# Kernel tuning notes

Hardware: AMD Instinct MI355X
Metric: run time of the kernel (lower is better)

Reference implementation:

```python
import jax, jax.numpy as jnp
import numpy as np
from jax import lax

B = 16384
T = 16

def _lin(x, w, b):
    return x @ w.T + b

def setup_inputs() -> dict:
    key = jax.random.key(0)
    ks = jax.random.split(key, 24)
    d = {
        'x': jax.random.normal(ks[0], (T, B, 64), jnp.float32),
        'cue': jax.random.uniform(ks[1], (B,), jnp.float32),
        'hc1': jax.random.normal(ks[2], (B, 256), jnp.float32),
        'hc2': jax.random.normal(ks[3], (B, 256), jnp.float32),
        'hc3': jax.random.normal(ks[4], (B, 256), jnp.float32),
        'hc4': jax.random.normal(ks[5], (B, 256), jnp.float32),
    }
    def w(k, o, i):
        return jax.random.normal(k, (o, i), jnp.float32) * 0.05
    def b(k, o):
        return jax.random.normal(k, (o,), jnp.float32) * 0.05
    d.update({
        'w1_i2h': w(ks[6], 256, 64),  'b1_i2h': b(ks[7], 256),
        'w1_h2h': w(ks[8], 256, 256), 'b1_h2h': b(ks[9], 256),
        'w1_h2o': w(ks[10], 64, 256), 'b1_h2o': b(ks[11], 64),
        'w2_i2h': w(ks[12], 256, 64), 'b2_i2h': b(ks[13], 256),
        'w2_h2h': w(ks[14], 256, 256),'b2_h2h': b(ks[15], 256),
        'w2_h2o': w(ks[16], 64, 256), 'b2_h2o': b(ks[17], 64),
        'w3_i2h': w(ks[18], 256, 130),'b3_i2h': b(ks[19], 256),
        'w3_h2h': w(ks[20], 256, 256),'b3_h2h': b(ks[21], 256),
        'w3_h2o': w(ks[22], 64, 256), 'b3_h2o': b(ks[23], 64),
        'w_fc': jax.random.normal(jax.random.fold_in(key, 100), (2, 64), jnp.float32) * 0.05,
        'b_fc': jax.random.normal(jax.random.fold_in(key, 101), (2,), jnp.float32) * 0.05,
    })
    return d

def reference(x, cue, hc1, hc2, hc3, hc4,
              w1_i2h, b1_i2h, w1_h2h, b1_h2h, w1_h2o, b1_h2o,
              w2_i2h, b2_i2h, w2_h2h, b2_h2h, w2_h2o, b2_h2o,
              w3_i2h, b3_i2h, w3_h2h, b3_h2h, w3_h2o, b3_h2o,
              w_fc, b_fc):
    # cue channels are identical at every timestep
    cue_step = jnp.stack([cue * 10.0, 10.0 * jnp.abs(cue - 1.0)], axis=-1)  # [B,2]
    cue_arr = jnp.broadcast_to(cue_step, (T,) + cue_step.shape)             # [T,B,2]

    def step(carry, xt):
        h1, h2, h3 = carry
        h1 = jnp.tanh(_lin(xt, w1_i2h, b1_i2h) + _lin(h1, w1_h2h, b1_h2h))
        o1 = jnp.tanh(_lin(h1, w1_h2o, b1_h2o))
        h2 = jnp.tanh(_lin(xt, w2_i2h, b2_i2h) + _lin(h2, w2_h2h, b2_h2h))
        o2 = jnp.tanh(_lin(h2, w2_h2o, b2_h2o))
        mid = jnp.concatenate([cue_step, o1, o2], axis=-1)  # [B,130]
        h3 = jnp.tanh(_lin(mid, w3_i2h, b3_i2h) + _lin(h3, w3_h2h, b3_h2h))
        of = jax.nn.relu(_lin(h3, w3_h2o, b3_h2o))
        y = _lin(of, w_fc, b_fc)
        return (h1, h2, h3), (y, o1, o2, of)

    (h1, h2, h3), (ys, o1s, o2s, ofs) = lax.scan(step, (hc1, hc2, hc3), x)
    # feed1_arr/feed2_arr are torch.empty (never written); use zeros as deterministic stand-in
    feed = jnp.zeros((T, x.shape[1], 256), dtype=x.dtype)
    return (ys, h1, h2, h3, hc4, o1s, o2s, cue_arr, feed, feed, ofs)
```

## Files before the change

### kernel.cpp

```cpp
#include <hip/hip_runtime.h>
#include <stdint.h>
#include <stddef.h>


#define BN 16384
#define TT 16

typedef short s16x8 __attribute__((ext_vector_type(8)));
typedef short s16x4 __attribute__((ext_vector_type(4)));
typedef float f32x4 __attribute__((ext_vector_type(4)));

#define MFMA(a, b, c) __builtin_amdgcn_mfma_f32_16x16x32_bf16((a), (b), (c), 0, 0, 0)
#define BARL() asm volatile("s_waitcnt lgkmcnt(0)\n\ts_barrier" ::: "memory")

__device__ __forceinline__ short f2bf(float f) {
  union { float f; uint32_t u; } v; v.f = f;
  uint32_t u = v.u;
  u += 0x7FFFu + ((u >> 16) & 1u);
  return (short)(u >> 16);
}
__device__ __forceinline__ float bf2f(short s) {
  union { uint32_t u; float f; } v; v.u = ((uint32_t)(uint16_t)s) << 16;
  return v.f;
}
__device__ __forceinline__ float fast_tanh(float xx) {
  float x = fminf(8.f, fmaxf(-8.f, xx));
  float e = __expf(2.f * x);
  return (e - 1.f) * __builtin_amdgcn_rcpf(e + 1.f);
}
__device__ __forceinline__ void nt_st4(float* p, f32x4 v) {
  __builtin_nontemporal_store(v, (f32x4*)p);
}
__device__ __forceinline__ f32x4 nt_ld4(const float* p) {
  return __builtin_nontemporal_load((const f32x4*)p);
}

struct PrepPtrs {
  const float *w1i, *w1h, *w1o, *w2i, *w2h, *w2o, *w3i, *w3h, *w3o;
  const float *b1i, *b1h, *b2i, *b2h, *b3i, *b3h, *bo1, *bo2, *bo3, *wfc, *bfc;
};

__global__ void prep_kernel(PrepPtrs pp, short* __restrict__ wpk, float* __restrict__ wmisc) {
  const float* P[9] = {pp.w1i, pp.w1h, pp.w1o, pp.w2i, pp.w2h, pp.w2o, pp.w3i, pp.w3h, pp.w3o};
  const int LD_[9] = {64, 256, 256, 64, 256, 256, 130, 256, 256};
  const int C0_[9] = {0, 0, 0, 0, 0, 0, 2, 0, 0};
  const int NT_[9] = {16, 16, 4, 16, 16, 4, 16, 16, 4};
  const int DO_[10] = {0, 16384, 81920, 98304, 114688, 180224, 196608, 229376, 294912, 311296};
  int stride = gridDim.x * blockDim.x;
  for (int g = blockIdx.x * blockDim.x + threadIdx.x; g < 311296; g += stride) {
    int m = 0;
    while (g >= DO_[m + 1]) ++m;
    int p = g - DO_[m];
    int NT = NT_[m];
    int frag = p >> 9, lane = (p >> 3) & 63, e = p & 7;
    int kt = frag / NT, nt = frag - kt * NT;
    int row = nt * 16 + (lane & 15);
    int col = kt * 32 + ((lane >> 4) << 3) + e;
    wpk[g] = f2bf(P[m][(size_t)row * LD_[m] + C0_[m] + col]);
  }
  for (int i = blockIdx.x * blockDim.x + threadIdx.x; i < 1602; i += stride) {
    float v;
    if      (i < 256)  v = pp.b1i[i]         + pp.b1h[i];
    else if (i < 512)  v = pp.b2i[i - 256]   + pp.b2h[i - 256];
    else if (i < 768)  v = pp.b3i[i - 512]   + pp.b3h[i - 512];
    else if (i < 832)  v = pp.bo1[i - 768];
    else if (i < 896)  v = pp.bo2[i - 832];
    else if (i < 960)  v = pp.bo3[i - 896];
    else if (i < 1088) v = pp.wfc[i - 960];
    else if (i < 1090) v = pp.bfc[i - 1088];
    else if (i < 1346) v = pp.w3i[(size_t)(i - 1090) * 130];
    else               v = pp.w3i[(size_t)(i - 1346) * 130 + 1];
    wmisc[i] = v;
  }
}

__launch_bounds__(512, 2)
__global__ void rnn_main(const float* __restrict__ x, const float* __restrict__ cue,
                         const float* __restrict__ hc1, const float* __restrict__ hc2,
                         const float* __restrict__ hc3, const float* __restrict__ hc4,
                         const short* __restrict__ wpk, const float* __restrict__ wmisc,
                         float* __restrict__ out) {
  __shared__ __align__(16) char pool[141312];
  short* h1s  = (short*)pool;
  short* h2s  = (short*)(pool + 32768);
  short* h3s  = (short*)(pool + 65536);
  short* o12s = (short*)(pool + 98304);
  float* ofl  = (float*)(pool + 114688);
  short* hscr = (short*)(pool + 98304);
  short* xls  = (short*)(pool + 133120);
  __shared__ float cue0[64], cue1[64];
  __shared__ __align__(16) float misc[1604];

  const int tid = threadIdx.x;
  const int wv = tid >> 6;
  const int lane = tid & 63;
  const int lr = lane & 15;
  const int lq = lane >> 4;
  const int swz = (lr & 7) << 3;
  const int r0 = blockIdx.x * 64;

  float* out_ys  = out;
  float* out_h1  = out + 524288;
  float* out_h2  = out + 4718592;
  float* out_h3  = out + 8912896;
  float* out_h4  = out + 13107200;
  float* out_o1s = out + 17301504;
  float* out_o2s = out + 34078720;
  float* out_cue = out + 50855936;
  float* out_f1  = out + 51380224;
  float* out_f2  = out + 118489088;
  float* out_of  = out + 185597952;

  for (int i = tid; i < 1602; i += 512) misc[i] = wmisc[i];
  if (tid < 64) {
    float cv = cue[r0 + tid];
    cue0[tid] = cv * 10.f;
    cue1[tid] = 10.f * fabsf(cv - 1.f);
  }
  for (int i = tid; i < 4096; i += 512) {
    int r = i >> 6, c0 = (i & 63) << 2;
    int li = r * 256 + (c0 ^ ((r & 7) << 3));
    size_t g = (size_t)(r0 + r) * 256 + c0;
    f32x4 v1 = __builtin_nontemporal_load((const f32x4*)(hc1 + g));
    f32x4 v2 = __builtin_nontemporal_load((const f32x4*)(hc2 + g));
    f32x4 v3 = __builtin_nontemporal_load((const f32x4*)(hc3 + g));
    f32x4 v4 = __builtin_nontemporal_load((const f32x4*)(hc4 + g));
    *(s16x4*)&h1s[li] = (s16x4){f2bf(v1.x), f2bf(v1.y), f2bf(v1.z), f2bf(v1.w)};
    *(s16x4*)&h2s[li] = (s16x4){f2bf(v2.x), f2bf(v2.y), f2bf(v2.z), f2bf(v2.w)};
    *(s16x4*)&h3s[li] = (s16x4){f2bf(v3.x), f2bf(v3.y), f2bf(v3.z), f2bf(v3.w)};
    nt_st4(out_h4 + g, v4);
  }
  const int xr = tid >> 3, xcq = (tid & 7) << 3;
  {
    const float* px = x + ((size_t)(r0 + xr)) * 64 + xcq;
    f32x4 a0 = nt_ld4(px);
    f32x4 a1 = nt_ld4(px + 4);
    *(s16x8*)&xls[xr * 64 + (xcq ^ ((xr & 7) << 3))] =
        (s16x8){f2bf(a0.x), f2bf(a0.y), f2bf(a0.z), f2bf(a0.w),
                f2bf(a1.x), f2bf(a1.y), f2bf(a1.z), f2bf(a1.w)};
  }
  __syncthreads();

  const short* Wp1i  = wpk;
  const short* Wp1h  = wpk + 16384;
  const short* Wp1o  = wpk + 81920;
  const short* Wp2i  = wpk + 98304;
  const short* Wp2h  = wpk + 114688;
  const short* Wp2o  = wpk + 180224;
  const short* Wp3ab = wpk + 196608;
  const short* Wp3h  = wpk + 229376;
  const short* Wp3o  = wpk + 294912;
  const float* bh1v = misc;
  const float* bh2v = misc + 256;
  const float* bh3v = misc + 512;
  const float* bo1v = misc + 768;
  const float* bo2v = misc + 832;
  const float* bofv = misc + 896;
  const float* wfcv = misc + 960;
  const float* bfcv = misc + 1088;
  const float* w3c0 = misc + 1090;
  const float* w3c1 = misc + 1346;

  for (int t = 0; t < TT; ++t) {
    BARL();

    {
      f32x4 acc1[4][2];
      #pragma unroll
      for (int j = 0; j < 2; ++j) {
        int nb = (2 * wv + j) * 16 + lq * 4;
        f32x4 b1 = *(const f32x4*)(bh1v + nb);
        #pragma unroll
        for (int rt = 0; rt < 4; ++rt) acc1[rt][j] = b1;
      }
      #pragma unroll
      for (int kt = 0; kt < 2; ++kt) {
        s16x8 aw0 = *(const s16x8*)(Wp1i + ((size_t)(kt * 16 + 2 * wv) * 64 + lane) * 8);
        s16x8 aw1 = *(const s16x8*)(Wp1i + ((size_t)(kt * 16 + 2 * wv + 1) * 64 + lane) * 8);
        #pragma unroll
        for (int rt = 0; rt < 4; ++rt) {
          s16x8 xb = *(const s16x8*)&xls[(rt * 16 + lr) * 64 + ((kt * 32 + lq * 8) ^ swz)];
          acc1[rt][0] = MFMA(aw0, xb, acc1[rt][0]);
          acc1[rt][1] = MFMA(aw1, xb, acc1[rt][1]);
        }
      }
      #pragma unroll
      for (int kt = 0; kt < 8; ++kt) {
        s16x8 aw0 = *(const s16x8*)(Wp1h + ((size_t)(kt * 16 + 2 * wv) * 64 + lane) * 8);
        s16x8 aw1 = *(const s16x8*)(Wp1h + ((size_t)(kt * 16 + 2 * wv + 1) * 64 + lane) * 8);
        #pragma unroll
        for (int rt = 0; rt < 4; ++rt) {
          s16x8 hb = *(const s16x8*)&h1s[(rt * 16 + lr) * 256 + ((kt * 32 + lq * 8) ^ swz)];
          acc1[rt][0] = MFMA(aw0, hb, acc1[rt][0]);
          acc1[rt][1] = MFMA(aw1, hb, acc1[rt][1]);
        }
      }
      #pragma unroll
      for (int j = 0; j < 2; ++j) {
        int cb = (2 * wv + j) * 16 + lq * 4;
        #pragma unroll
        for (int rt = 0; rt < 4; ++rt) {
          *(s16x4*)&hscr[(rt * 16 + lr) * 256 + (cb ^ swz)] =
              (s16x4){f2bf(fast_tanh(acc1[rt][j][0])), f2bf(fast_tanh(acc1[rt][j][1])),
                      f2bf(fast_tanh(acc1[rt][j][2])), f2bf(fast_tanh(acc1[rt][j][3]))};
        }
      }
    }

    {
      f32x4 acc2[4][2];
      #pragma unroll
      for (int j = 0; j < 2; ++j) {
        int nb = (2 * wv + j) * 16 + lq * 4;
        f32x4 b2 = *(const f32x4*)(bh2v + nb);
        #pragma unroll
        for (int rt = 0; rt < 4; ++rt) acc2[rt][j] = b2;
      }
      #pragma unroll
      for (int kt = 0; kt < 2; ++kt) {
        s16x8 aw0 = *(const s16x8*)(Wp2i + ((size_t)(kt * 16 + 2 * wv) * 64 + lane) * 8);
        s16x8 aw1 = *(const s16x8*)(Wp2i + ((size_t)(kt * 16 + 2 * wv + 1) * 64 + lane) * 8);
        #pragma unroll
        for (int rt = 0; rt < 4; ++rt) {
          s16x8 xb = *(const s16x8*)&xls[(rt * 16 + lr) * 64 + ((kt * 32 + lq * 8) ^ swz)];
          acc2[rt][0] = MFMA(aw0, xb, acc2[rt][0]);
          acc2[rt][1] = MFMA(aw1, xb, acc2[rt][1]);
        }
      }
      #pragma unroll
      for (int kt = 0; kt < 8; ++kt) {
        s16x8 aw0 = *(const s16x8*)(Wp2h + ((size_t)(kt * 16 + 2 * wv) * 64 + lane) * 8);
        s16x8 aw1 = *(const s16x8*)(Wp2h + ((size_t)(kt * 16 + 2 * wv + 1) * 64 + lane) * 8);
        #pragma unroll
        for (int rt = 0; rt < 4; ++rt) {
          s16x8 hb = *(const s16x8*)&h2s[(rt * 16 + lr) * 256 + ((kt * 32 + lq * 8) ^ swz)];
          acc2[rt][0] = MFMA(aw0, hb, acc2[rt][0]);
          acc2[rt][1] = MFMA(aw1, hb, acc2[rt][1]);
        }
      }
      __syncthreads();
      #pragma unroll
      for (int j = 0; j < 2; ++j) {
        int cb = (2 * wv + j) * 16 + lq * 4;
        #pragma unroll
        for (int rt = 0; rt < 4; ++rt) {
          *(s16x4*)&h2s[(rt * 16 + lr) * 256 + (cb ^ swz)] =
              (s16x4){f2bf(fast_tanh(acc2[rt][j][0])), f2bf(fast_tanh(acc2[rt][j][1])),
                      f2bf(fast_tanh(acc2[rt][j][2])), f2bf(fast_tanh(acc2[rt][j][3]))};
        }
      }
      #pragma unroll
      for (int i = 0; i < 4; ++i) {
        int e = (i * 512 + tid) * 8;
        *(s16x8*)&h1s[e] = *(const s16x8*)&hscr[e];
      }
      __syncthreads();
    }

    {
      int cell = wv >> 2, w4 = wv & 3;
      const short* hs = cell ? h2s : h1s;
      const short* Wo = cell ? Wp2o : Wp1o;
      const float* bo = cell ? bo2v : bo1v;
      int nb = w4 * 16 + lq * 4;
      f32x4 bb = *(const f32x4*)(bo + nb);
      f32x4 acc[4];
      #pragma unroll
      for (int rt = 0; rt < 4; ++rt) acc[rt] = bb;
      #pragma unroll
      for (int kt = 0; kt < 8; ++kt) {
        s16x8 aw = *(const s16x8*)(Wo + ((size_t)(kt * 4 + w4) * 64 + lane) * 8);
        #pragma unroll
        for (int rt = 0; rt < 4; ++rt) {
          s16x8 hb = *(const s16x8*)&hs[(rt * 16 + lr) * 256 + ((kt * 32 + lq * 8) ^ swz)];
          acc[rt] = MFMA(aw, hb, acc[rt]);
        }
      }
      int cb = cell * 64 + nb;
      #pragma unroll
      for (int rt = 0; rt < 4; ++rt) {
        *(s16x4*)&o12s[(rt * 16 + lr) * 128 + (cb ^ swz)] =
            (s16x4){f2bf(fast_tanh(acc[rt][0])), f2bf(fast_tanh(acc[rt][1])),
                    f2bf(fast_tanh(acc[rt][2])), f2bf(fast_tanh(acc[rt][3]))};
      }
    }
    __syncthreads();

    {
      f32x4 acc3[4][2];
      #pragma unroll
      for (int j = 0; j < 2; ++j) {
        int nb = (2 * wv + j) * 16 + lq * 4;
        f32x4 bb  = *(const f32x4*)(bh3v + nb);
        f32x4 c0w = *(const f32x4*)(w3c0 + nb);
        f32x4 c1w = *(const f32x4*)(w3c1 + nb);
        #pragma unroll
        for (int rt = 0; rt < 4; ++rt) {
          float cz = cue0[rt * 16 + lr], co = cue1[rt * 16 + lr];
          acc3[rt][j] = bb + cz * c0w + co * c1w;
        }
      }
      #pragma unroll
      for (int kt = 0; kt < 4; ++kt) {
        s16x8 aw0 = *(const s16x8*)(Wp3ab + ((size_t)(kt * 16 + 2 * wv) * 64 + lane) * 8);
        s16x8 aw1 = *(const s16x8*)(Wp3ab + ((size_t)(kt * 16 + 2 * wv + 1) * 64 + lane) * 8);
        #pragma unroll
        for (int rt = 0; rt < 4; ++rt) {
          s16x8 ob = *(const s16x8*)&o12s[(rt * 16 + lr) * 128 + ((kt * 32 + lq * 8) ^ swz)];
          acc3[rt][0] = MFMA(aw0, ob, acc3[rt][0]);
          acc3[rt][1] = MFMA(aw1, ob, acc3[rt][1]);
        }
      }
      #pragma unroll
      for (int kt = 0; kt < 8; ++kt) {
        s16x8 aw0 = *(const s16x8*)(Wp3h + ((size_t)(kt * 16 + 2 * wv) * 64 + lane) * 8);
        s16x8 aw1 = *(const s16x8*)(Wp3h + ((size_t)(kt * 16 + 2 * wv + 1) * 64 + lane) * 8);
        #pragma unroll
        for (int rt = 0; rt < 4; ++rt) {
          s16x8 hb = *(const s16x8*)&h3s[(rt * 16 + lr) * 256 + ((kt * 32 + lq * 8) ^ swz)];
          acc3[rt][0] = MFMA(aw0, hb, acc3[rt][0]);
          acc3[rt][1] = MFMA(aw1, hb, acc3[rt][1]);
        }
      }
      __syncthreads();
      #pragma unroll
      for (int j = 0; j < 2; ++j) {
        int cb = (2 * wv + j) * 16 + lq * 4;
        #pragma unroll
        for (int rt = 0; rt < 4; ++rt) {
          *(s16x4*)&h3s[(rt * 16 + lr) * 256 + (cb ^ swz)] =
              (s16x4){f2bf(fast_tanh(acc3[rt][j][0])), f2bf(fast_tanh(acc3[rt][j][1])),
                      f2bf(fast_tanh(acc3[rt][j][2])), f2bf(fast_tanh(acc3[rt][j][3]))};
        }
      }
      __syncthreads();
    }

    int tn = (t + 1 < TT) ? (t + 1) : t;
    const float* pxn = x + ((size_t)tn * BN + r0 + xr) * 64 + xcq;
    f32x4 xa0 = nt_ld4(pxn);
    f32x4 xa1 = nt_ld4(pxn + 4);

    if (wv < 4) {
      int nb = wv * 16 + lq * 4;
      f32x4 bb = *(const f32x4*)(bofv + nb);
      f32x4 acc[4];
      #pragma unroll
      for (int rt = 0; rt < 4; ++rt) acc[rt] = bb;
      #pragma unroll
      for (int kt = 0; kt < 8; ++kt) {
        s16x8 aw = *(const s16x8*)(Wp3o + ((size_t)(kt * 4 + wv) * 64 + lane) * 8);
        #pragma unroll
        for (int rt = 0; rt < 4; ++rt) {
          s16x8 hb = *(const s16x8*)&h3s[(rt * 16 + lr) * 256 + ((kt * 32 + lq * 8) ^ swz)];
          acc[rt] = MFMA(aw, hb, acc[rt]);
        }
      }
      #pragma unroll
      for (int rt = 0; rt < 4; ++rt) {
        f32x4 v = (f32x4){fmaxf(0.f, acc[rt][0]), fmaxf(0.f, acc[rt][1]),
                          fmaxf(0.f, acc[rt][2]), fmaxf(0.f, acc[rt][3])};
        *(f32x4*)&ofl[(rt * 16 + lr) * 72 + nb] = v;
      }
    } else {
      size_t ob = ((size_t)t * BN + r0) * 64;
      float* targ = (wv < 6) ? out_o1s : out_o2s;
      int coff = (wv < 6) ? 0 : 64;
      int wq = wv & 1;
      #pragma unroll
      for (int s = 0; s < 8; ++s) {
        int f = wq * 2048 + s * 256 + lane * 4;
        int r = f >> 6, c = f & 63;
        s16x4 v = *(const s16x4*)&o12s[r * 128 + ((c + coff) ^ ((r & 7) << 3))];
        nt_st4(targ + ob + f, (f32x4){bf2f(v[0]), bf2f(v[1]), bf2f(v[2]), bf2f(v[3])});
      }
    }
    BARL();

    {
      size_t ob = ((size_t)t * BN + r0) * 64;
      int r = tid >> 3, c0 = (tid & 7) << 3;
      nt_st4(out_of + ob + r * 64 + c0,     *(const f32x4*)&ofl[r * 72 + c0]);
      nt_st4(out_of + ob + r * 64 + c0 + 4, *(const f32x4*)&ofl[r * 72 + c0 + 4]);
      *(s16x8*)&xls[xr * 64 + (xcq ^ ((xr & 7) << 3))] =
          (s16x8){f2bf(xa0.x), f2bf(xa0.y), f2bf(xa0.z), f2bf(xa0.w),
                  f2bf(xa1.x), f2bf(xa1.y), f2bf(xa1.z), f2bf(xa1.w)};
      if (tid < 128) {
        int rr = tid >> 1, jj = tid & 1;
        const f32x4* wr4 = (const f32x4*)(wfcv + jj * 64);
        const f32x4* or4 = (const f32x4*)&ofl[rr * 72];
        f32x4 sv = (f32x4){0.f, 0.f, 0.f, 0.f};
        #pragma unroll
        for (int kk = 0; kk < 16; ++kk) sv += or4[kk] * wr4[kk];
        float s = bfcv[jj] + sv[0] + sv[1] + sv[2] + sv[3];
        size_t yi = ((size_t)t * BN + r0 + rr) * 2 + jj;
        __builtin_nontemporal_store(s, out_ys + yi);
        __builtin_nontemporal_store(jj ? cue1[rr] : cue0[rr], out_cue + yi);
      }
      size_t fb = ((size_t)t * BN + r0) * 256;
      f32x4 z = (f32x4){0.f, 0.f, 0.f, 0.f};
      #pragma unroll
      for (int s = 0; s < 8; ++s) {
        nt_st4(out_f1 + fb + (size_t)(s * 512 + tid) * 4, z);
        nt_st4(out_f2 + fb + (size_t)(s * 512 + tid) * 4, z);
      }
    }
  }

  for (int i = tid; i < 4096; i += 512) {
    int r = i >> 6, c0 = (i & 63) << 2;
    int li = r * 256 + (c0 ^ ((r & 7) << 3));
    size_t g = (size_t)(r0 + r) * 256 + c0;
    s16x4 s1 = *(const s16x4*)&h1s[li];
    s16x4 s2 = *(const s16x4*)&h2s[li];
    s16x4 s3 = *(const s16x4*)&h3s[li];
    nt_st4(out_h1 + g, (f32x4){bf2f(s1[0]), bf2f(s1[1]), bf2f(s1[2]), bf2f(s1[3])});
    nt_st4(out_h2 + g, (f32x4){bf2f(s2[0]), bf2f(s2[1]), bf2f(s2[2]), bf2f(s2[3])});
    nt_st4(out_h3 + g, (f32x4){bf2f(s3[0]), bf2f(s3[1]), bf2f(s3[2]), bf2f(s3[3])});
  }
}

extern "C" void kernel_launch(void* const* d_in, const int* in_sizes, int n_in,
                              void* d_out, int out_size, void* d_ws, size_t ws_size,
                              hipStream_t stream) {
  const float* x   = (const float*)d_in[0];
  const float* cue = (const float*)d_in[1];
  const float* hc1 = (const float*)d_in[2];
  const float* hc2 = (const float*)d_in[3];
  const float* hc3 = (const float*)d_in[4];
  const float* hc4 = (const float*)d_in[5];
  PrepPtrs pp;
  pp.w1i = (const float*)d_in[6];  pp.b1i = (const float*)d_in[7];
  pp.w1h = (const float*)d_in[8];  pp.b1h = (const float*)d_in[9];
  pp.w1o = (const float*)d_in[10]; pp.bo1 = (const float*)d_in[11];
  pp.w2i = (const float*)d_in[12]; pp.b2i = (const float*)d_in[13];
  pp.w2h = (const float*)d_in[14]; pp.b2h = (const float*)d_in[15];
  pp.w2o = (const float*)d_in[16]; pp.bo2 = (const float*)d_in[17];
  pp.w3i = (const float*)d_in[18]; pp.b3i = (const float*)d_in[19];
  pp.w3h = (const float*)d_in[20]; pp.b3h = (const float*)d_in[21];
  pp.w3o = (const float*)d_in[22]; pp.bo3 = (const float*)d_in[23];
  pp.wfc = (const float*)d_in[24]; pp.bfc = (const float*)d_in[25];

  short* wpk   = (short*)d_ws;
  float* wmisc = (float*)((char*)d_ws + 622592);

  prep_kernel<<<64, 256, 0, stream>>>(pp, wpk, wmisc);
  rnn_main<<<256, 512, 0, stream>>>(x, cue, hc1, hc2, hc3, hc4, wpk, wmisc, (float*)d_out);
}
```

Before: 524.5 us.

## Fuse h3 recurrent GEMM into o1/o2 stage and drop a barrier

Moves the h3·W3h recurrent matmul, which depends only on the previous h3, into the o1/o2 output-projection loop so both run in one pass and interleave MFMAs. This removes one __syncthreads per timestep and lets the cell-3 stage finish with only the short input-projection part. It also simplifies tanh to a single-rcp form and uses the HIP bf16 conversion intrinsic, which may compile to hardware conversion. The tanh rewrite drops the lower clamp, so it relies on exp underflow behaving well for very negative inputs.

```diff
diff --git a/kernel.cpp b/kernel.cpp
--- a/kernel.cpp
+++ b/kernel.cpp
@@ -1,4 +1,5 @@
 #include <hip/hip_runtime.h>
+#include <hip/hip_bf16.h>
 #include <stdint.h>
 #include <stddef.h>
 
@@ -14,25 +15,28 @@
 #define BARL() asm volatile("s_waitcnt lgkmcnt(0)\n\ts_barrier" ::: "memory")
 
 __device__ __forceinline__ short f2bf(float f) {
-  union { float f; uint32_t u; } v; v.f = f;
-  uint32_t u = v.u;
-  u += 0x7FFFu + ((u >> 16) & 1u);
-  return (short)(u >> 16);
+  __hip_bfloat16 h = __float2bfloat16(f);
+  short s;
+  __builtin_memcpy(&s, &h, 2);
+  return s;
 }
 __device__ __forceinline__ float bf2f(short s) {
   union { uint32_t u; float f; } v; v.u = ((uint32_t)(uint16_t)s) << 16;
   return v.f;
 }
-__device__ __forceinline__ float fast_tanh(float xx) {
-  float x = fminf(8.f, fmaxf(-8.f, xx));
-  float e = __expf(2.f * x);
-  return (e - 1.f) * __builtin_amdgcn_rcpf(e + 1.f);
+__device__ __forceinline__ float fast_tanh(float x) {
+  float e = __expf(2.f * fminf(x, 8.f));
+  return 1.f - 2.f * __builtin_amdgcn_rcpf(e + 1.f);
 }
 __device__ __forceinline__ void nt_st4(float* p, f32x4 v) {
   __builtin_nontemporal_store(v, (f32x4*)p);
 }
 __device__ __forceinline__ f32x4 nt_ld4(const float* p) {
   return __builtin_nontemporal_load((const f32x4*)p);
+}
+__device__ __forceinline__ s16x4 tanh4bf(f32x4 a) {
+  return (s16x4){f2bf(fast_tanh(a[0])), f2bf(fast_tanh(a[1])),
+                 f2bf(fast_tanh(a[2])), f2bf(fast_tanh(a[3]))};
 }
 
 struct PrepPtrs {
@@ -125,9 +129,9 @@
     f32x4 v2 = __builtin_nontemporal_load((const f32x4*)(hc2 + g));
     f32x4 v3 = __builtin_nontemporal_load((const f32x4*)(hc3 + g));
     f32x4 v4 = __builtin_nontemporal_load((const f32x4*)(hc4 + g));
-    *(s16x4*)&h1s[li] = (s16x4){f2bf(v1.x), f2bf(v1.y), f2bf(v1.z), f2bf(v1.w)};
-    *(s16x4*)&h2s[li] = (s16x4){f2bf(v2.x), f2bf(v2.y), f2bf(v2.z), f2bf(v2.w)};
-    *(s16x4*)&h3s[li] = (s16x4){f2bf(v3.x), f2bf(v3.y), f2bf(v3.z), f2bf(v3.w)};
+    *(s16x4*)&h1s[li] = (s16x4){f2bf(v1[0]), f2bf(v1[1]), f2bf(v1[2]), f2bf(v1[3])};
+    *(s16x4*)&h2s[li] = (s16x4){f2bf(v2[0]), f2bf(v2[1]), f2bf(v2[2]), f2bf(v2[3])};
+    *(s16x4*)&h3s[li] = (s16x4){f2bf(v3[0]), f2bf(v3[1]), f2bf(v3[2]), f2bf(v3[3])};
     nt_st4(out_h4 + g, v4);
   }
   const int xr = tid >> 3, xcq = (tid & 7) << 3;
@@ -136,8 +140,8 @@
     f32x4 a0 = nt_ld4(px);
     f32x4 a1 = nt_ld4(px + 4);
     *(s16x8*)&xls[xr * 64 + (xcq ^ ((xr & 7) << 3))] =
-        (s16x8){f2bf(a0.x), f2bf(a0.y), f2bf(a0.z), f2bf(a0.w),
-                f2bf(a1.x), f2bf(a1.y), f2bf(a1.z), f2bf(a1.w)};
+        (s16x8){f2bf(a0[0]), f2bf(a0[1]), f2bf(a0[2]), f2bf(a0[3]),
+                f2bf(a1[0]), f2bf(a1[1]), f2bf(a1[2]), f2bf(a1[3])};
   }
   __syncthreads();
 
@@ -199,11 +203,8 @@
       for (int j = 0; j < 2; ++j) {
         int cb = (2 * wv + j) * 16 + lq * 4;
         #pragma unroll
-        for (int rt = 0; rt < 4; ++rt) {
-          *(s16x4*)&hscr[(rt * 16 + lr) * 256 + (cb ^ swz)] =
-              (s16x4){f2bf(fast_tanh(acc1[rt][j][0])), f2bf(fast_tanh(acc1[rt][j][1])),
-                      f2bf(fast_tanh(acc1[rt][j][2])), f2bf(fast_tanh(acc1[rt][j][3]))};
-        }
+        for (int rt = 0; rt < 4; ++rt)
+          *(s16x4*)&hscr[(rt * 16 + lr) * 256 + (cb ^ swz)] = tanh4bf(acc1[rt][j]);
       }
     }
 
@@ -243,11 +244,8 @@
       for (int j = 0; j < 2; ++j) {
         int cb = (2 * wv + j) * 16 + lq * 4;
         #pragma unroll
-        for (int rt = 0; rt < 4; ++rt) {
-          *(s16x4*)&h2s[(rt * 16 + lr) * 256 + (cb ^ swz)] =
-              (s16x4){f2bf(fast_tanh(acc2[rt][j][0])), f2bf(fast_tanh(acc2[rt][j][1])),
-                      f2bf(fast_tanh(acc2[rt][j][2])), f2bf(fast_tanh(acc2[rt][j][3]))};
-        }
+        for (int rt = 0; rt < 4; ++rt)
+          *(s16x4*)&h2s[(rt * 16 + lr) * 256 + (cb ^ swz)] = tanh4bf(acc2[rt][j]);
       }
       #pragma unroll
       for (int i = 0; i < 4; ++i) {
@@ -257,49 +255,51 @@
       __syncthreads();
     }
 
+    f32x4 acc3[4][2];
     {
+      #pragma unroll
+      for (int j = 0; j < 2; ++j) {
+        int nb = (2 * wv + j) * 16 + lq * 4;
+        f32x4 bb  = *(const f32x4*)(bh3v + nb);
+        f32x4 c0w = *(const f32x4*)(w3c0 + nb);
+        f32x4 c1w = *(const f32x4*)(w3c1 + nb);
+        #pragma unroll
+        for (int rt = 0; rt < 4; ++rt) {
+          float cz = cue0[rt * 16 + lr], co = cue1[rt * 16 + lr];
+          acc3[rt][j] = bb + cz * c0w + co * c1w;
+        }
+      }
       int cell = wv >> 2, w4 = wv & 3;
       const short* hs = cell ? h2s : h1s;
       const short* Wo = cell ? Wp2o : Wp1o;
       const float* bo = cell ? bo2v : bo1v;
       int nb = w4 * 16 + lq * 4;
       f32x4 bb = *(const f32x4*)(bo + nb);
-      f32x4 acc[4];
-      #pragma unroll
-      for (int rt = 0; rt < 4; ++rt) acc[rt] = bb;
+      f32x4 acco[4];
+      #pragma unroll
+      for (int rt = 0; rt < 4; ++rt) acco[rt] = bb;
       #pragma unroll
       for (int kt = 0; kt < 8; ++kt) {
-        s16x8 aw = *(const s16x8*)(Wo + ((size_t)(kt * 4 + w4) * 64 + lane) * 8);
-        #pragma unroll
-        for (int rt = 0; rt < 4; ++rt) {
-          s16x8 hb = *(const s16x8*)&hs[(rt * 16 + lr) * 256 + ((kt * 32 + lq * 8) ^ swz)];
-          acc[rt] = MFMA(aw, hb, acc[rt]);
+        s16x8 aw0 = *(const s16x8*)(Wp3h + ((size_t)(kt * 16 + 2 * wv) * 64 + lane) * 8);
+        s16x8 aw1 = *(const s16x8*)(Wp3h + ((size_t)(kt * 16 + 2 * wv + 1) * 64 + lane) * 8);
+        s16x8 awo = *(const s16x8*)(Wo + ((size_t)(kt * 4 + w4) * 64 + lane) * 8);
+        #pragma unroll
+        for (int rt = 0; rt < 4; ++rt) {
+          s16x8 hb3 = *(const s16x8*)&h3s[(rt * 16 + lr) * 256 + ((kt * 32 + lq * 8) ^ swz)];
+          s16x8 hbo = *(const s16x8*)&hs[(rt * 16 + lr) * 256 + ((kt * 32 + lq * 8) ^ swz)];
+          acc3[rt][0] = MFMA(aw0, hb3, acc3[rt][0]);
+          acc3[rt][1] = MFMA(aw1, hb3, acc3[rt][1]);
+          acco[rt] = MFMA(awo, hbo, acco[rt]);
         }
       }
       int cb = cell * 64 + nb;
       #pragma unroll
-      for (int rt = 0; rt < 4; ++rt) {
-        *(s16x4*)&o12s[(rt * 16 + lr) * 128 + (cb ^ swz)] =
-            (s16x4){f2bf(fast_tanh(acc[rt][0])), f2bf(fast_tanh(acc[rt][1])),
-                    f2bf(fast_tanh(acc[rt][2])), f2bf(fast_tanh(acc[rt][3]))};
-      }
+      for (int rt = 0; rt < 4; ++rt)
+        *(s16x4*)&o12s[(rt * 16 + lr) * 128 + (cb ^ swz)] = tanh4bf(acco[rt]);
     }
     __syncthreads();
 
     {
-      f32x4 acc3[4][2];
-      #pragma unroll
-      for (int j = 0; j < 2; ++j) {
-        int nb = (2 * wv + j) * 16 + lq * 4;
-        f32x4 bb  = *(const f32x4*)(bh3v + nb);
-        f32x4 c0w = *(const f32x4*)(w3c0 + nb);
-        f32x4 c1w = *(const f32x4*)(w3c1 + nb);
-        #pragma unroll
-        for (int rt = 0; rt < 4; ++rt) {
-          float cz = cue0[rt * 16 + lr], co = cue1[rt * 16 + lr];
-          acc3[rt][j] = bb + cz * c0w + co * c1w;
-        }
-      }
       #pragma unroll
       for (int kt = 0; kt < 4; ++kt) {
         s16x8 aw0 = *(const s16x8*)(Wp3ab + ((size_t)(kt * 16 + 2 * wv) * 64 + lane) * 8);
@@ -312,29 +312,14 @@
         }
       }
       #pragma unroll
-      for (int kt = 0; kt < 8; ++kt) {
-        s16x8 aw0 = *(const s16x8*)(Wp3h + ((size_t)(kt * 16 + 2 * wv) * 64 + lane) * 8);
-        s16x8 aw1 = *(const s16x8*)(Wp3h + ((size_t)(kt * 16 + 2 * wv + 1) * 64 + lane) * 8);
-        #pragma unroll
-        for (int rt = 0; rt < 4; ++rt) {
-          s16x8 hb = *(const s16x8*)&h3s[(rt * 16 + lr) * 256 + ((kt * 32 + lq * 8) ^ swz)];
-          acc3[rt][0] = MFMA(aw0, hb, acc3[rt][0]);
-          acc3[rt][1] = MFMA(aw1, hb, acc3[rt][1]);
-        }
-      }
-      __syncthreads();
-      #pragma unroll
       for (int j = 0; j < 2; ++j) {
         int cb = (2 * wv + j) * 16 + lq * 4;
         #pragma unroll
-        for (int rt = 0; rt < 4; ++rt) {
-          *(s16x4*)&h3s[(rt * 16 + lr) * 256 + (cb ^ swz)] =
-              (s16x4){f2bf(fast_tanh(acc3[rt][j][0])), f2bf(fast_tanh(acc3[rt][j][1])),
-                      f2bf(fast_tanh(acc3[rt][j][2])), f2bf(fast_tanh(acc3[rt][j][3]))};
-        }
-      }
-      __syncthreads();
-    }
+        for (int rt = 0; rt < 4; ++rt)
+          *(s16x4*)&h3s[(rt * 16 + lr) * 256 + (cb ^ swz)] = tanh4bf(acc3[rt][j]);
+      }
+    }
+    __syncthreads();
 
     int tn = (t + 1 < TT) ? (t + 1) : t;
     const float* pxn = x + ((size_t)tn * BN + r0 + xr) * 64 + xcq;
@@ -383,8 +368,8 @@
       nt_st4(out_of + ob + r * 64 + c0,     *(const f32x4*)&ofl[r * 72 + c0]);
       nt_st4(out_of + ob + r * 64 + c0 + 4, *(const f32x4*)&ofl[r * 72 + c0 + 4]);
       *(s16x8*)&xls[xr * 64 + (xcq ^ ((xr & 7) << 3))] =
-          (s16x8){f2bf(xa0.x), f2bf(xa0.y), f2bf(xa0.z), f2bf(xa0.w),
-                  f2bf(xa1.x), f2bf(xa1.y), f2bf(xa1.z), f2bf(xa1.w)};
+          (s16x8){f2bf(xa0[0]), f2bf(xa0[1]), f2bf(xa0[2]), f2bf(xa0[3]),
+                  f2bf(xa1[0]), f2bf(xa1[1]), f2bf(xa1[2]), f2bf(xa1[3])};
       if (tid < 128) {
         int rr = tid >> 1, jj = tid & 1;
         const f32x4* wr4 = (const f32x4*)(wfcv + jj * 64);
```

Result: slower. 631.7 us (+20.4%).
